# Kernel tuning notes

Hardware: AMD Instinct MI355X
Metric: run time of the kernel (lower is better)

Reference implementation:

```python
import jax, jax.numpy as jnp
import numpy as np
import math

B, LL, LP = 16, 256, 1024
HID, H = 128, 8
SCALE = math.sqrt(HID)


def setup_inputs() -> dict:
    key = jax.random.key(0)
    ks = jax.random.split(key, 20)
    s = 0.02
    inp = {
        "ligand": jax.random.normal(ks[0], (B, LL, HID), jnp.float32),
        "prot": jax.random.normal(ks[1], (B, LP, HID), jnp.float32),
        "inter": jax.random.uniform(ks[2], (B, 1, LL, LP), jnp.float32),
        # projection weights stored as [in, out] (x @ W + b)
        "Wl1": jax.random.normal(ks[3], (HID, HID * H), jnp.float32) * s,
        "bl1": jnp.zeros((HID * H,), jnp.float32),
        "Wl2": jax.random.normal(ks[4], (HID, HID * H), jnp.float32) * s,
        "bl2": jnp.zeros((HID * H,), jnp.float32),
        "Wp1": jax.random.normal(ks[5], (HID, HID * H), jnp.float32) * s,
        "bp1": jnp.zeros((HID * H,), jnp.float32),
        "Wp2": jax.random.normal(ks[6], (HID, HID * H), jnp.float32) * s,
        "bp2": jnp.zeros((HID * H,), jnp.float32),
        "W11": jax.random.normal(ks[7], (HID * H, HID), jnp.float32) * s,
        "b11": jnp.zeros((HID,), jnp.float32),
        "W12": jax.random.normal(ks[8], (2 * HID, HID), jnp.float32) * s,
        "b12": jnp.zeros((HID,), jnp.float32),
        "W21": jax.random.normal(ks[9], (HID * H, HID), jnp.float32) * s,
        "b21": jnp.zeros((HID,), jnp.float32),
        "W22": jax.random.normal(ks[10], (2 * HID, HID), jnp.float32) * s,
        "b22": jnp.zeros((HID,), jnp.float32),
    }
    return inp


def _heads(x):
    # [B, L, H*D] -> [B, H, L, D]
    b, l, _ = x.shape
    return x.reshape(b, l, H, HID).transpose(0, 2, 1, 3)


def reference(ligand, prot, inter, Wl1, bl1, Wl2, bl2, Wp1, bp1, Wp2, bp2,
              W11, b11, W12, b12, W21, b21, W22, b22):
    relu = jax.nn.relu
    l1 = _heads(relu(ligand @ Wl1 + bl1))   # [B,H,LL,D]
    l2 = _heads(relu(ligand @ Wl2 + bl2))   # [B,H,LL,D]
    p1 = _heads(relu(prot @ Wp1 + bp1))     # [B,H,LP,D]
    p2 = _heads(relu(prot @ Wp2 + bp2))     # [B,H,LP,D]

    energy = jnp.einsum('bhld,bhpd->bhlp', l1, p1) / SCALE
    att = jax.nn.softmax(energy * inter, axis=-1)  # dropout is identity at eval

    # ligand branch: att @ prot2 -> [B,LL,H*D]
    lig3 = jnp.einsum('bhlp,bhpd->blhd', att, p2).reshape(B, LL, H * HID)
    lig3 = jnp.concatenate([lig3 @ W11 + b11, ligand], axis=2)
    lig3 = relu(lig3 @ W12 + b12)

    # protein branch: att^T @ ligand2 -> [B,LP,H*D]
    prot3 = jnp.einsum('bhlp,bhld->bphd', att, l2).reshape(B, LP, H * HID)
    prot3 = jnp.concatenate([prot3 @ W21 + b21, prot], axis=2)
    prot3 = relu(prot3 @ W22 + b22)
    return (lig3, prot3)
```

## Files before the change

### kernel.cpp

```cpp
#include <hip/hip_runtime.h>
#include <hip/hip_bf16.h>

typedef unsigned short u16;
typedef __attribute__((ext_vector_type(4))) float f32x4;
typedef __attribute__((ext_vector_type(4))) unsigned int u32x4;
typedef __attribute__((ext_vector_type(4))) unsigned short u16x4;
typedef __attribute__((ext_vector_type(8))) __bf16 bf16x8;

__device__ inline float u2f(u16 u) {
    union { unsigned int i; float f; } x; x.i = ((unsigned int)u) << 16; return x.f;
}
__device__ inline u16 f2u(float f) {
    __hip_bfloat16 b = __float2bfloat16(f);
    return *reinterpret_cast<u16*>(&b);
}
__device__ inline f32x4 mfma16(bf16x8 a, bf16x8 b, f32x4 c) {
    return __builtin_amdgcn_mfma_f32_16x16x32_bf16(a, b, c, 0, 0, 0);
}
__device__ inline void gload_lds16(const u16* g, u16* l) {
    __builtin_amdgcn_global_load_lds(
        (const __attribute__((address_space(1))) unsigned int*)g,
        (__attribute__((address_space(3))) unsigned int*)l, 16, 0, 0);
}

__global__ __launch_bounds__(256)
void proj_kernel(const u16* __restrict__ ligb, const u16* __restrict__ protb,
                 const u16* __restrict__ Wl1t, const u16* __restrict__ Wl2t,
                 const u16* __restrict__ Wp1t, const u16* __restrict__ Wp2t,
                 const float* __restrict__ bl1, const float* __restrict__ bl2,
                 const float* __restrict__ bp1, const float* __restrict__ bp2,
                 u16* __restrict__ l1v, u16* __restrict__ l2tv,
                 u16* __restrict__ p1v, u16* __restrict__ p2tv)
{
    __shared__ __align__(16) u16 As[128 * 64];
    __shared__ __align__(16) u16 Bs[128 * 64];
    const int y = blockIdx.y;
    const u16* A; const u16* B; const float* bias; u16* Out;
    int mode, logL, my;
    if (y < 32)       { A = ligb;  B = Wl1t; bias = bl1; Out = l1v;  mode = 1; logL = 8;  my = y; }
    else if (y < 64)  { A = ligb;  B = Wl2t; bias = bl2; Out = l2tv; mode = 3; logL = 8;  my = y - 32; }
    else if (y < 192) { A = protb; B = Wp1t; bias = bp1; Out = p1v;  mode = 1; logL = 10; my = y - 64; }
    else              { A = protb; B = Wp2t; bias = bp2; Out = p2tv; mode = 3; logL = 10; my = y - 192; }
    const int n0 = blockIdx.x * 128, m0 = my * 128;
    const int tid = threadIdx.x;
    const int w = tid >> 6, lane = tid & 63, q = lane >> 4, li = lane & 15;
    const int wr = w >> 1, wc = w & 1;

    const int srow = tid >> 3;
    const int cg = (tid & 7) ^ (srow & 7);
    const int ldsbase = ((tid >> 6) * 8) * 64;

    f32x4 acc[4][4];
    #pragma unroll
    for (int i = 0; i < 4; i++)
        #pragma unroll
        for (int j = 0; j < 4; j++) acc[i][j] = (f32x4){0.f, 0.f, 0.f, 0.f};

    #pragma unroll
    for (int kt = 0; kt < 128; kt += 64) {
        const u16* Ab = A + (long)m0 * 128 + kt + cg * 8;
        const u16* Bb = B + (long)n0 * 128 + kt + cg * 8;
        #pragma unroll
        for (int c = 0; c < 4; c++) {
            gload_lds16(Ab + (long)(c * 32 + srow) * 128, &As[ldsbase + c * 32 * 64]);
            gload_lds16(Bb + (long)(c * 32 + srow) * 128, &Bs[ldsbase + c * 32 * 64]);
        }
        __syncthreads();
        #pragma unroll
        for (int s = 0; s < 2; s++) {
            const int cp = ((s * 4 + q) ^ (li & 7)) * 8;
            bf16x8 av[4], bv[4];
            #pragma unroll
            for (int i = 0; i < 4; i++)
                av[i] = *(bf16x8*)&As[(wr * 64 + i * 16 + li) * 64 + cp];
            #pragma unroll
            for (int j = 0; j < 4; j++)
                bv[j] = *(bf16x8*)&Bs[(wc * 64 + j * 16 + li) * 64 + cp];
            #pragma unroll
            for (int i = 0; i < 4; i++)
                #pragma unroll
                for (int j = 0; j < 4; j++)
                    acc[i][j] = mfma16(av[i], bv[j], acc[i][j]);
        }
        __syncthreads();
    }

    const int Lm = (1 << logL) - 1;
    #pragma unroll
    for (int i = 0; i < 4; i++) {
        #pragma unroll
        for (int j = 0; j < 4; j++) {
            const int col = n0 + wc * 64 + j * 16 + li;
            const float bvs = bias[col];
            if (mode == 3) {
                const int row0 = m0 + wr * 64 + i * 16 + q * 4;
                long base = ((long)(((row0 >> logL) * 8 + (col >> 7)) * 128
                            + (col & 127)) << logL) + (row0 & Lm);
                u16x4 o;
                #pragma unroll
                for (int r = 0; r < 4; r++)
                    o[r] = f2u(fmaxf(acc[i][j][r] + bvs, 0.f));
                *(u16x4*)(Out + base) = o;
            } else {
                #pragma unroll
                for (int r = 0; r < 4; r++) {
                    const int row = m0 + wr * 64 + i * 16 + q * 4 + r;
                    long addr = ((long)((row >> logL) * 8 + (col >> 7)) << (logL + 7))
                              + ((long)(row & Lm) << 7) + (col & 127);
                    Out[addr] = f2u(fmaxf(acc[i][j][r] + bvs, 0.f));
                }
            }
        }
    }
}

__global__ __launch_bounds__(512)
void av_kernel(const u16* __restrict__ att, const u16* __restrict__ p2t,
               const u16* __restrict__ l2t,
               u16* __restrict__ lig3, u16* __restrict__ prot3)
{
    __shared__ __align__(16) u16 As[256 * 64];
    __shared__ __align__(16) u16 Bs[128 * 64];
    __shared__ __align__(16) u16 T[64 * 256];
    const int bid = blockIdx.x;
    const int tid = threadIdx.x;
    const int w = tid >> 6, lane = tid & 63, q = lane >> 4, li = lane & 15;
    const int wr = w >> 1, wc = w & 1;

    f32x4 acc[4][4];
    #pragma unroll
    for (int i = 0; i < 4; i++)
        #pragma unroll
        for (int j = 0; j < 4; j++) acc[i][j] = (f32x4){0.f, 0.f, 0.f, 0.f};

    if (bid < 128) {
        const int bh = bid;
        const u16* A = att + (long)bh * 262144;
        const u16* B = p2t + (long)bh * 131072;
        const int srow = tid >> 3;
        const int cg = (tid & 7) ^ (srow & 7);
        const int ldsbase = ((tid >> 6) * 8) * 64;

        for (int kt = 0; kt < 1024; kt += 64) {
            const u16* Ab = A + kt + cg * 8;
            const u16* Bb = B + kt + cg * 8;
            #pragma unroll
            for (int c = 0; c < 4; c++)
                gload_lds16(Ab + (long)(c * 64 + srow) * 1024,
                            &As[ldsbase + c * 64 * 64]);
            #pragma unroll
            for (int c = 0; c < 2; c++)
                gload_lds16(Bb + (long)(c * 64 + srow) * 1024,
                            &Bs[ldsbase + c * 64 * 64]);
            __syncthreads();
            #pragma unroll
            for (int s = 0; s < 2; s++) {
                const int cp = ((s * 4 + q) ^ (li & 7)) * 8;
                bf16x8 av[4], bv[4];
                #pragma unroll
                for (int i = 0; i < 4; i++)
                    av[i] = *(bf16x8*)&As[(wr * 64 + i * 16 + li) * 64 + cp];
                #pragma unroll
                for (int j = 0; j < 4; j++)
                    bv[j] = *(bf16x8*)&Bs[(wc * 64 + j * 16 + li) * 64 + cp];
                #pragma unroll
                for (int i = 0; i < 4; i++)
                    #pragma unroll
                    for (int j = 0; j < 4; j++)
                        acc[i][j] = mfma16(av[i], bv[j], acc[i][j]);
            }
            __syncthreads();
        }

        const long obase = ((long)(bh >> 3) * 256) * 1024 + (long)(bh & 7) * 128;
        #pragma unroll
        for (int i = 0; i < 4; i++)
            #pragma unroll
            for (int j = 0; j < 4; j++) {
                const int col = wc * 64 + j * 16 + li;
                #pragma unroll
                for (int r = 0; r < 4; r++) {
                    const int row = wr * 64 + i * 16 + q * 4 + r;
                    lig3[obase + (long)row * 1024 + col] = f2u(acc[i][j][r]);
                }
            }
    } else {
        const int pb = bid - 128;
        const int bh = pb >> 2;
        const int m0 = (pb & 3) * 256;
        const u16* A = att + (long)bh * 262144;
        const u16* B = l2t + (long)bh * 32768;
        const int w6 = tid >> 6;
        const int i5 = (tid >> 5) & 1;
        const int srow = tid >> 3;
        const int cg = (tid & 7) ^ (srow & 7);
        const int bldsbase = w6 * 8 * 64;

        for (int kt = 0; kt < 256; kt += 64) {
            #pragma unroll
            for (int c = 0; c < 4; c++) {
                gload_lds16(A + (long)(kt + w6 * 8 + c * 2 + i5) * 1024
                              + m0 + (tid & 31) * 8,
                            &T[w6 * 2048 + c * 512]);
            }
            #pragma unroll
            for (int c = 0; c < 2; c++)
                gload_lds16(B + (long)(c * 64 + srow) * 256 + kt + cg * 8,
                            &Bs[bldsbase + c * 64 * 64]);
            __syncthreads();

            #pragma unroll
            for (int pass = 0; pass < 4; pass++) {
                const int p = pass * 64 + (tid & 63);
                union { u16 e[8]; u32x4 v; } tmp;
                #pragma unroll
                for (int e = 0; e < 8; e++)
                    tmp.e[e] = T[(w6 * 8 + e) * 256 + p];
                *(u32x4*)&As[p * 64 + ((w6 ^ (p & 7)) * 8)] = tmp.v;
            }
            __syncthreads();

            #pragma unroll
            for (int s = 0; s < 2; s++) {
                const int cp = ((s * 4 + q) ^ (li & 7)) * 8;
                bf16x8 av[4], bv[4];
                #pragma unroll
                for (int i = 0; i < 4; i++)
                    av[i] = *(bf16x8*)&As[(wr * 64 + i * 16 + li) * 64 + cp];
                #pragma unroll
                for (int j = 0; j < 4; j++)
                    bv[j] = *(bf16x8*)&Bs[(wc * 64 + j * 16 + li) * 64 + cp];
                #pragma unroll
                for (int i = 0; i < 4; i++)
                    #pragma unroll
                    for (int j = 0; j < 4; j++)
                        acc[i][j] = mfma16(av[i], bv[j], acc[i][j]);
            }
            __syncthreads();
        }

        const long obase = ((long)(bh >> 3) * 1024 + m0) * 1024 + (long)(bh & 7) * 128;
        #pragma unroll
        for (int i = 0; i < 4; i++)
            #pragma unroll
            for (int j = 0; j < 4; j++) {
                const int col = wc * 64 + j * 16 + li;
                #pragma unroll
                for (int r = 0; r < 4; r++) {
                    const int row = wr * 64 + i * 16 + q * 4 + r;
                    prot3[obase + (long)row * 1024 + col] = f2u(acc[i][j][r]);
                }
            }
    }
}

__global__ __launch_bounds__(256)
void finals_kernel(const u16* __restrict__ lig3, const u16* __restrict__ ligb,
                   const u16* __restrict__ WstL, const float* __restrict__ bcL,
                   float* __restrict__ out0,
                   const u16* __restrict__ prot3, const u16* __restrict__ protb,
                   const u16* __restrict__ WstP, const float* __restrict__ bcP,
                   float* __restrict__ out1)
{
    __shared__ __align__(16) u16 As[128 * 64];
    __shared__ __align__(16) u16 Bs[128 * 64];
    const int y = blockIdx.y;
    const u16 *A, *A2, *B; const float* bias; float* Out; int my;
    if (y < 32) { A = lig3;  A2 = ligb;  B = WstL; bias = bcL; Out = out0; my = y; }
    else        { A = prot3; A2 = protb; B = WstP; bias = bcP; Out = out1; my = y - 32; }
    const int m0 = my * 128;
    const int tid = threadIdx.x;
    const int w = tid >> 6, lane = tid & 63, q = lane >> 4, li = lane & 15;
    const int wr = w >> 1, wc = w & 1;

    const int srow = tid >> 3;
    const int cg = (tid & 7) ^ (srow & 7);
    const int ldsbase = ((tid >> 6) * 8) * 64;

    f32x4 acc[4][4];
    #pragma unroll
    for (int i = 0; i < 4; i++)
        #pragma unroll
        for (int j = 0; j < 4; j++) acc[i][j] = (f32x4){0.f, 0.f, 0.f, 0.f};

    for (int kt = 0; kt < 1152; kt += 64) {
        const u16* Abase; long lda; int ktA;
        if (kt >= 1024) { Abase = A2; lda = 128; ktA = kt - 1024; }
        else            { Abase = A;  lda = 1024; ktA = kt; }
        const u16* Ab = Abase + (long)m0 * lda + ktA + cg * 8;
        const u16* Bb = B + kt + cg * 8;
        #pragma unroll
        for (int c = 0; c < 4; c++) {
            gload_lds16(Ab + (long)(c * 32 + srow) * lda,  &As[ldsbase + c * 32 * 64]);
            gload_lds16(Bb + (long)(c * 32 + srow) * 1152, &Bs[ldsbase + c * 32 * 64]);
        }
        __syncthreads();
        #pragma unroll
        for (int s = 0; s < 2; s++) {
            const int cp = ((s * 4 + q) ^ (li & 7)) * 8;
            bf16x8 av[4], bv[4];
            #pragma unroll
            for (int i = 0; i < 4; i++)
                av[i] = *(bf16x8*)&As[(wr * 64 + i * 16 + li) * 64 + cp];
            #pragma unroll
            for (int j = 0; j < 4; j++)
                bv[j] = *(bf16x8*)&Bs[(wc * 64 + j * 16 + li) * 64 + cp];
            #pragma unroll
            for (int i = 0; i < 4; i++)
                #pragma unroll
                for (int j = 0; j < 4; j++)
                    acc[i][j] = mfma16(av[i], bv[j], acc[i][j]);
        }
        __syncthreads();
    }

    #pragma unroll
    for (int i = 0; i < 4; i++)
        #pragma unroll
        for (int j = 0; j < 4; j++) {
            const int col = wc * 64 + j * 16 + li;
            const float bvs = bias[col];
            #pragma unroll
            for (int r = 0; r < 4; r++) {
                const int row = m0 + wr * 64 + i * 16 + q * 4 + r;
                Out[(long)row * 128 + col] = fmaxf(acc[i][j][r] + bvs, 0.f);
            }
        }
}

__global__ __launch_bounds__(256)
void attn_kernel(const u16* __restrict__ l1, const u16* __restrict__ p1,
                 const float* __restrict__ inter, u16* __restrict__ att)
{
    __shared__ __align__(16) u16 As[16][136];
    __shared__ float wmax[4][16];
    __shared__ float wsum[4][16];
    const int bh = blockIdx.y;
    const int b  = bh >> 3;
    const int m0 = blockIdx.x * 16;
    const int tid = threadIdx.x;
    const int w = tid >> 6, lane = tid & 63, q = lane >> 4, li = lane & 15;

    {
        const int row = tid >> 4, col = (tid & 15) * 8;
        *(u32x4*)&As[row][col] =
            *(const u32x4*)(l1 + ((long)bh * 256 + m0 + row) * 128 + col);
    }
    __syncthreads();

    bf16x8 af[4];
    #pragma unroll
    for (int s = 0; s < 4; s++) af[s] = *(bf16x8*)&As[li][s * 32 + q * 8];

    float sv[16][4];
    const float rscale = 0.08838834764831845f;
    for (int t = 0; t < 16; t++) {
        const int n0 = w * 256 + t * 16;
        const u16* bp = p1 + ((long)bh * 1024 + n0 + li) * 128 + q * 8;
        f32x4 acc = (f32x4){0.f, 0.f, 0.f, 0.f};
        #pragma unroll
        for (int s = 0; s < 4; s++) {
            bf16x8 bfg = *(const bf16x8*)(bp + s * 32);
            acc = mfma16(af[s], bfg, acc);
        }
        const int pcol = n0 + li;
        #pragma unroll
        for (int r = 0; r < 4; r++) {
            const int l = m0 + q * 4 + r;
            float iv = inter[((long)b * 256 + l) * 1024 + pcol];
            sv[t][r] = acc[r] * rscale * iv;
        }
    }

    float rmax[4];
    #pragma unroll
    for (int r = 0; r < 4; r++) {
        float m = sv[0][r];
        #pragma unroll
        for (int t = 1; t < 16; t++) m = fmaxf(m, sv[t][r]);
        for (int d = 1; d < 16; d <<= 1) m = fmaxf(m, __shfl_xor(m, d, 64));
        rmax[r] = m;
    }
    if (li == 0) {
        #pragma unroll
        for (int r = 0; r < 4; r++) wmax[w][q * 4 + r] = rmax[r];
    }
    __syncthreads();
    float gmax[4];
    #pragma unroll
    for (int r = 0; r < 4; r++) {
        gmax[r] = fmaxf(fmaxf(wmax[0][q * 4 + r], wmax[1][q * 4 + r]),
                        fmaxf(wmax[2][q * 4 + r], wmax[3][q * 4 + r]));
    }
    #pragma unroll
    for (int r = 0; r < 4; r++) {
        float s = 0.f;
        #pragma unroll
        for (int t = 0; t < 16; t++) {
            float e = __expf(sv[t][r] - gmax[r]);
            sv[t][r] = e;
            s += e;
        }
        for (int d = 1; d < 16; d <<= 1) s += __shfl_xor(s, d, 64);
        if (li == 0) wsum[w][q * 4 + r] = s;
    }
    __syncthreads();
    float inv[4];
    #pragma unroll
    for (int r = 0; r < 4; r++) {
        float s = wsum[0][q * 4 + r] + wsum[1][q * 4 + r]
                + wsum[2][q * 4 + r] + wsum[3][q * 4 + r];
        inv[r] = 1.f / s;
    }
    for (int t = 0; t < 16; t++) {
        #pragma unroll
        for (int r = 0; r < 4; r++) {
            const int l = m0 + q * 4 + r;
            const int pcol = w * 256 + t * 16 + li;
            att[((long)bh * 256 + l) * 1024 + pcol] = f2u(sv[t][r] * inv[r]);
        }
    }
}

struct TPF { const float* src; u16* dst; int R; int C; };
struct TPF8 { TPF t[8]; };

__global__ __launch_bounds__(256)
void cvtw_kernel(TPF8 args)
{
    TPF tp = args.t[blockIdx.z];
    const int c0 = blockIdx.x * 32, r0 = blockIdx.y * 32;
    if (c0 >= tp.C || r0 >= tp.R) return;
    __shared__ u16 tile[32][33];
    const int tx = threadIdx.x & 31, ty = threadIdx.x >> 5;
    #pragma unroll
    for (int i = 0; i < 4; i++)
        tile[ty + i * 8][tx] = f2u(tp.src[(long)(r0 + ty + i * 8) * tp.C + c0 + tx]);
    __syncthreads();
    #pragma unroll
    for (int i = 0; i < 4; i++)
        tp.dst[(long)(c0 + ty + i * 8) * tp.R + r0 + tx] = tile[tx][ty + i * 8];
}

__global__ __launch_bounds__(256)
void wcomb_kernel(const u16* __restrict__ Wm0, const u16* __restrict__ Wo0,
                  const float* __restrict__ bm0, const float* __restrict__ bo0,
                  u16* __restrict__ Wst0, float* __restrict__ bc0,
                  const u16* __restrict__ Wm1, const u16* __restrict__ Wo1,
                  const float* __restrict__ bm1, const float* __restrict__ bo1,
                  u16* __restrict__ Wst1, float* __restrict__ bc1)
{
    const int zz = blockIdx.y;
    const u16* Wm = zz ? Wm1 : Wm0;
    const u16* Wo = zz ? Wo1 : Wo0;
    const float* bmid = zz ? bm1 : bm0;
    const float* bout = zz ? bo1 : bo0;
    u16* Wst = zz ? Wst1 : Wst0;
    float* bc = zz ? bc1 : bc0;
    const int n = blockIdx.x;
    const int tid = threadIdx.x;
    __shared__ float wrow[128];
    if (tid < 128) wrow[tid] = u2f(Wo[n * 256 + tid]);
    __syncthreads();
    for (int k = tid; k < 1024; k += 256) {
        float acc = 0.f;
        #pragma unroll 4
        for (int j = 0; j < 128; j++) acc += wrow[j] * u2f(Wm[(long)j * 1024 + k]);
        Wst[(long)n * 1152 + k] = f2u(acc);
    }
    if (tid < 128) Wst[(long)n * 1152 + 1024 + tid] = Wo[n * 256 + 128 + tid];
    if (tid == 0) {
        float acc = bout[n];
        for (int j = 0; j < 128; j++) acc += bmid[j] * wrow[j];
        bc[n] = acc;
    }
}

__global__ __launch_bounds__(256)
void cvt2_kernel(const float* __restrict__ a, u16* __restrict__ da, int na,
                 const float* __restrict__ b, u16* __restrict__ db, int nb)
{
    const int zz = blockIdx.y;
    const float* s = zz ? b : a;
    u16* d = zz ? db : da;
    const int n = zz ? nb : na;
    const int i = (blockIdx.x * 256 + threadIdx.x) * 4;
    if (i >= n) return;
    const float4 v = *(const float4*)(s + i);
    u16x4 o;
    o.x = f2u(v.x); o.y = f2u(v.y); o.z = f2u(v.z); o.w = f2u(v.w);
    *(u16x4*)(d + i) = o;
}

extern "C" void kernel_launch(void* const* d_in, const int* in_sizes, int n_in,
                              void* d_out, int out_size, void* d_ws, size_t ws_size,
                              hipStream_t stream)
{
    (void)in_sizes; (void)n_in; (void)out_size; (void)ws_size;
    const float* ligand = (const float*)d_in[0];
    const float* prot   = (const float*)d_in[1];
    const float* inter  = (const float*)d_in[2];
    const float* Wl1 = (const float*)d_in[3];  const float* bl1 = (const float*)d_in[4];
    const float* Wl2 = (const float*)d_in[5];  const float* bl2 = (const float*)d_in[6];
    const float* Wp1 = (const float*)d_in[7];  const float* bp1 = (const float*)d_in[8];
    const float* Wp2 = (const float*)d_in[9];  const float* bp2 = (const float*)d_in[10];
    const float* W11 = (const float*)d_in[11]; const float* b11 = (const float*)d_in[12];
    const float* W12 = (const float*)d_in[13]; const float* b12 = (const float*)d_in[14];
    const float* W21 = (const float*)d_in[15]; const float* b21 = (const float*)d_in[16];
    const float* W22 = (const float*)d_in[17]; const float* b22 = (const float*)d_in[18];

    float* out0 = (float*)d_out;
    float* out1 = out0 + (size_t)16 * 256 * 128;

    u16* ws = (u16*)d_ws;
    size_t off = 0;
    auto alloc = [&](size_t n) { u16* p = ws + off; off += n; return p; };
    u16* ligb  = alloc(524288);
    u16* protb = alloc(2097152);
    u16* l1v   = alloc(4194304);
    u16* l2t   = alloc(4194304);
    u16* p1v   = alloc(16777216);
    u16* p2t   = alloc(16777216);
    u16* attv  = alloc(33554432);
    u16* lig3  = alloc(4194304);
    u16* prot3 = alloc(16777216);
    u16* Wl1t  = alloc(131072);
    u16* Wl2t  = alloc(131072);
    u16* Wp1t  = alloc(131072);
    u16* Wp2t  = alloc(131072);
    u16* W11t  = alloc(131072);
    u16* W21t  = alloc(131072);
    u16* W12t  = alloc(32768);
    u16* W22t  = alloc(32768);
    u16* WstL  = alloc(147456);
    u16* WstP  = alloc(147456);
    float* bcL = (float*)alloc(256);
    float* bcP = (float*)alloc(256);

    cvt2_kernel<<<dim3(2048, 2), 256, 0, stream>>>(
        ligand, ligb, 524288, prot, protb, 2097152);

    TPF8 tp;
    tp.t[0] = {Wl1, Wl1t, 128, 1024};
    tp.t[1] = {Wl2, Wl2t, 128, 1024};
    tp.t[2] = {Wp1, Wp1t, 128, 1024};
    tp.t[3] = {Wp2, Wp2t, 128, 1024};
    tp.t[4] = {W11, W11t, 1024, 128};
    tp.t[5] = {W21, W21t, 1024, 128};
    tp.t[6] = {W12, W12t, 256, 128};
    tp.t[7] = {W22, W22t, 256, 128};
    cvtw_kernel<<<dim3(32, 32, 8), 256, 0, stream>>>(tp);

    wcomb_kernel<<<dim3(128, 2), 256, 0, stream>>>(
        W11t, W12t, b11, b12, WstL, bcL,
        W21t, W22t, b21, b22, WstP, bcP);

    proj_kernel<<<dim3(8, 320), 256, 0, stream>>>(
        ligb, protb, Wl1t, Wl2t, Wp1t, Wp2t,
        bl1, bl2, bp1, bp2, l1v, l2t, p1v, p2t);

    attn_kernel<<<dim3(16, 128), 256, 0, stream>>>(l1v, p1v, inter, attv);

    av_kernel<<<dim3(640), 512, 0, stream>>>(attv, p2t, l2t, lig3, prot3);

    finals_kernel<<<dim3(1, 160), 256, 0, stream>>>(
        lig3, ligb, WstL, bcL, out0,
        prot3, protb, WstP, bcP, out1);
}
```

Before: 328.0 us.

## Reuse A tile across four N tiles in proj and widen attention blocks

The projection kernel now loads the full 128x128 A tile into LDS once and loops over four 128-column weight tiles, so A reloads are cut and the grid shrinks fourfold. The attention kernel processes 32 query rows per 512-thread block instead of 16 per 256, so each block covers more rows and p1 loads are shared by the two row groups through cache. In exchange, the projection grid has fewer blocks and each block runs a serial loop with syncs. LDS use also doubles, which may lower occupancy.

```diff
diff --git a/kernel.cpp b/kernel.cpp
--- a/kernel.cpp
+++ b/kernel.cpp
@@ -32,8 +32,8 @@
                  u16* __restrict__ l1v, u16* __restrict__ l2tv,
                  u16* __restrict__ p1v, u16* __restrict__ p2tv)
 {
-    __shared__ __align__(16) u16 As[128 * 64];
-    __shared__ __align__(16) u16 Bs[128 * 64];
+    __shared__ __align__(16) u16 As[2][128 * 64];
+    __shared__ __align__(16) u16 Bs[2][128 * 64];
     const int y = blockIdx.y;
     const u16* A; const u16* B; const float* bias; u16* Out;
     int mode, logL, my;
@@ -41,76 +41,89 @@
     else if (y < 64)  { A = ligb;  B = Wl2t; bias = bl2; Out = l2tv; mode = 3; logL = 8;  my = y - 32; }
     else if (y < 192) { A = protb; B = Wp1t; bias = bp1; Out = p1v;  mode = 1; logL = 10; my = y - 64; }
     else              { A = protb; B = Wp2t; bias = bp2; Out = p2tv; mode = 3; logL = 10; my = y - 192; }
-    const int n0 = blockIdx.x * 128, m0 = my * 128;
+    const int m0 = my * 128;
+    const int nbase = blockIdx.x * 512;
     const int tid = threadIdx.x;
     const int w = tid >> 6, lane = tid & 63, q = lane >> 4, li = lane & 15;
     const int wr = w >> 1, wc = w & 1;
 
     const int srow = tid >> 3;
-    const int cg = (tid & 7) ^ (srow & 7);
+    const int cgx = (tid & 7) ^ (srow & 7);
     const int ldsbase = ((tid >> 6) * 8) * 64;
 
-    f32x4 acc[4][4];
-    #pragma unroll
-    for (int i = 0; i < 4; i++)
-        #pragma unroll
-        for (int j = 0; j < 4; j++) acc[i][j] = (f32x4){0.f, 0.f, 0.f, 0.f};
-
-    #pragma unroll
-    for (int kt = 0; kt < 128; kt += 64) {
-        const u16* Ab = A + (long)m0 * 128 + kt + cg * 8;
-        const u16* Bb = B + (long)n0 * 128 + kt + cg * 8;
-        #pragma unroll
-        for (int c = 0; c < 4; c++) {
-            gload_lds16(Ab + (long)(c * 32 + srow) * 128, &As[ldsbase + c * 32 * 64]);
-            gload_lds16(Bb + (long)(c * 32 + srow) * 128, &Bs[ldsbase + c * 32 * 64]);
+    #pragma unroll
+    for (int h = 0; h < 2; h++) {
+        const u16* Ab = A + (long)m0 * 128 + h * 64 + cgx * 8;
+        #pragma unroll
+        for (int c = 0; c < 4; c++)
+            gload_lds16(Ab + (long)(c * 32 + srow) * 128, &As[h][ldsbase + c * 32 * 64]);
+    }
+
+    const int Lm = (1 << logL) - 1;
+    for (int nt = 0; nt < 4; nt++) {
+        const int n0 = nbase + nt * 128;
+        #pragma unroll
+        for (int h = 0; h < 2; h++) {
+            const u16* Bb = B + (long)n0 * 128 + h * 64 + cgx * 8;
+            #pragma unroll
+            for (int c = 0; c < 4; c++)
+                gload_lds16(Bb + (long)(c * 32 + srow) * 128, &Bs[h][ldsbase + c * 32 * 64]);
         }
         __syncthreads();
-        #pragma unroll
-        for (int s = 0; s < 2; s++) {
-            const int cp = ((s * 4 + q) ^ (li & 7)) * 8;
-            bf16x8 av[4], bv[4];
-            #pragma unroll
-            for (int i = 0; i < 4; i++)
-                av[i] = *(bf16x8*)&As[(wr * 64 + i * 16 + li) * 64 + cp];
-            #pragma unroll
-            for (int j = 0; j < 4; j++)
-                bv[j] = *(bf16x8*)&Bs[(wc * 64 + j * 16 + li) * 64 + cp];
-            #pragma unroll
-            for (int i = 0; i < 4; i++)
+
+        f32x4 acc[4][4];
+        #pragma unroll
+        for (int i = 0; i < 4; i++)
+            #pragma unroll
+            for (int j = 0; j < 4; j++) acc[i][j] = (f32x4){0.f, 0.f, 0.f, 0.f};
+
+        #pragma unroll
+        for (int h = 0; h < 2; h++) {
+            #pragma unroll
+            for (int s = 0; s < 2; s++) {
+                const int cp = ((s * 4 + q) ^ (li & 7)) * 8;
+                bf16x8 av[4], bv[4];
+                #pragma unroll
+                for (int i = 0; i < 4; i++)
+                    av[i] = *(bf16x8*)&As[h][(wr * 64 + i * 16 + li) * 64 + cp];
                 #pragma unroll
                 for (int j = 0; j < 4; j++)
-                    acc[i][j] = mfma16(av[i], bv[j], acc[i][j]);
+                    bv[j] = *(bf16x8*)&Bs[h][(wc * 64 + j * 16 + li) * 64 + cp];
+                #pragma unroll
+                for (int i = 0; i < 4; i++)
+                    #pragma unroll
+                    for (int j = 0; j < 4; j++)
+                        acc[i][j] = mfma16(av[i], bv[j], acc[i][j]);
+            }
+        }
+
+        #pragma unroll
+        for (int i = 0; i < 4; i++) {
+            #pragma unroll
+            for (int j = 0; j < 4; j++) {
+                const int col = n0 + wc * 64 + j * 16 + li;
+                const float bvs = bias[col];
+                if (mode == 3) {
+                    const int row0 = m0 + wr * 64 + i * 16 + q * 4;
+                    long base = ((long)(((row0 >> logL) * 8 + (col >> 7)) * 128
+                                + (col & 127)) << logL) + (row0 & Lm);
+                    u16x4 o;
+                    #pragma unroll
+                    for (int r = 0; r < 4; r++)
+                        o[r] = f2u(fmaxf(acc[i][j][r] + bvs, 0.f));
+                    *(u16x4*)(Out + base) = o;
+                } else {
+                    #pragma unroll
+                    for (int r = 0; r < 4; r++) {
+                        const int row = m0 + wr * 64 + i * 16 + q * 4 + r;
+                        long addr = ((long)((row >> logL) * 8 + (col >> 7)) << (logL + 7))
+                                  + ((long)(row & Lm) << 7) + (col & 127);
+                        Out[addr] = f2u(fmaxf(acc[i][j][r] + bvs, 0.f));
+                    }
+                }
+            }
         }
         __syncthreads();
-    }
-
-    const int Lm = (1 << logL) - 1;
-    #pragma unroll
-    for (int i = 0; i < 4; i++) {
-        #pragma unroll
-        for (int j = 0; j < 4; j++) {
-            const int col = n0 + wc * 64 + j * 16 + li;
-            const float bvs = bias[col];
-            if (mode == 3) {
-                const int row0 = m0 + wr * 64 + i * 16 + q * 4;
-                long base = ((long)(((row0 >> logL) * 8 + (col >> 7)) * 128
-                            + (col & 127)) << logL) + (row0 & Lm);
-                u16x4 o;
-                #pragma unroll
-                for (int r = 0; r < 4; r++)
-                    o[r] = f2u(fmaxf(acc[i][j][r] + bvs, 0.f));
-                *(u16x4*)(Out + base) = o;
-            } else {
-                #pragma unroll
-                for (int r = 0; r < 4; r++) {
-                    const int row = m0 + wr * 64 + i * 16 + q * 4 + r;
-                    long addr = ((long)((row >> logL) * 8 + (col >> 7)) << (logL + 7))
-                              + ((long)(row & Lm) << 7) + (col & 127);
-                    Out[addr] = f2u(fmaxf(acc[i][j][r] + bvs, 0.f));
-                }
-            }
-        }
     }
 }
 
@@ -328,18 +341,19 @@
         }
 }
 
-__global__ __launch_bounds__(256)
+__global__ __launch_bounds__(512)
 void attn_kernel(const u16* __restrict__ l1, const u16* __restrict__ p1,
                  const float* __restrict__ inter, u16* __restrict__ att)
 {
-    __shared__ __align__(16) u16 As[16][136];
-    __shared__ float wmax[4][16];
-    __shared__ float wsum[4][16];
+    __shared__ __align__(16) u16 As[32][136];
+    __shared__ float wmax[8][16];
+    __shared__ float wsum[8][16];
     const int bh = blockIdx.y;
     const int b  = bh >> 3;
-    const int m0 = blockIdx.x * 16;
+    const int m0 = blockIdx.x * 32;
     const int tid = threadIdx.x;
     const int w = tid >> 6, lane = tid & 63, q = lane >> 4, li = lane & 15;
+    const int rg = w >> 2, cg = w & 3;
 
     {
         const int row = tid >> 4, col = (tid & 15) * 8;
@@ -350,12 +364,12 @@
 
     bf16x8 af[4];
     #pragma unroll
-    for (int s = 0; s < 4; s++) af[s] = *(bf16x8*)&As[li][s * 32 + q * 8];
+    for (int s = 0; s < 4; s++) af[s] = *(bf16x8*)&As[rg * 16 + li][s * 32 + q * 8];
 
     float sv[16][4];
     const float rscale = 0.08838834764831845f;
     for (int t = 0; t < 16; t++) {
-        const int n0 = w * 256 + t * 16;
+        const int n0 = cg * 256 + t * 16;
         const u16* bp = p1 + ((long)bh * 1024 + n0 + li) * 128 + q * 8;
         f32x4 acc = (f32x4){0.f, 0.f, 0.f, 0.f};
         #pragma unroll
@@ -366,31 +380,26 @@
         const int pcol = n0 + li;
         #pragma unroll
         for (int r = 0; r < 4; r++) {
-            const int l = m0 + q * 4 + r;
+            const int l = m0 + rg * 16 + q * 4 + r;
             float iv = inter[((long)b * 256 + l) * 1024 + pcol];
             sv[t][r] = acc[r] * rscale * iv;
         }
     }
 
-    float rmax[4];
     #pragma unroll
     for (int r = 0; r < 4; r++) {
         float m = sv[0][r];
         #pragma unroll
         for (int t = 1; t < 16; t++) m = fmaxf(m, sv[t][r]);
         for (int d = 1; d < 16; d <<= 1) m = fmaxf(m, __shfl_xor(m, d, 64));
-        rmax[r] = m;
-    }
-    if (li == 0) {
-        #pragma unroll
-        for (int r = 0; r < 4; r++) wmax[w][q * 4 + r] = rmax[r];
+        if (li == 0) wmax[w][q * 4 + r] = m;
     }
     __syncthreads();
     float gmax[4];
     #pragma unroll
     for (int r = 0; r < 4; r++) {
-        gmax[r] = fmaxf(fmaxf(wmax[0][q * 4 + r], wmax[1][q * 4 + r]),
-                        fmaxf(wmax[2][q * 4 + r], wmax[3][q * 4 + r]));
+        gmax[r] = fmaxf(fmaxf(wmax[rg * 4 + 0][q * 4 + r], wmax[rg * 4 + 1][q * 4 + r]),
+                        fmaxf(wmax[rg * 4 + 2][q * 4 + r], wmax[rg * 4 + 3][q * 4 + r]));
     }
     #pragma unroll
     for (int r = 0; r < 4; r++) {
@@ -408,15 +417,15 @@
     float inv[4];
     #pragma unroll
     for (int r = 0; r < 4; r++) {
-        float s = wsum[0][q * 4 + r] + wsum[1][q * 4 + r]
-                + wsum[2][q * 4 + r] + wsum[3][q * 4 + r];
+        float s = wsum[rg * 4 + 0][q * 4 + r] + wsum[rg * 4 + 1][q * 4 + r]
+                + wsum[rg * 4 + 2][q * 4 + r] + wsum[rg * 4 + 3][q * 4 + r];
         inv[r] = 1.f / s;
     }
     for (int t = 0; t < 16; t++) {
         #pragma unroll
         for (int r = 0; r < 4; r++) {
-            const int l = m0 + q * 4 + r;
-            const int pcol = w * 256 + t * 16 + li;
+            const int l = m0 + rg * 16 + q * 4 + r;
+            const int pcol = cg * 256 + t * 16 + li;
             att[((long)bh * 256 + l) * 1024 + pcol] = f2u(sv[t][r] * inv[r]);
         }
     }
@@ -555,11 +564,11 @@
         W11t, W12t, b11, b12, WstL, bcL,
         W21t, W22t, b21, b22, WstP, bcP);
 
-    proj_kernel<<<dim3(8, 320), 256, 0, stream>>>(
+    proj_kernel<<<dim3(2, 320), 256, 0, stream>>>(
         ligb, protb, Wl1t, Wl2t, Wp1t, Wp2t,
         bl1, bl2, bp1, bp2, l1v, l2t, p1v, p2t);
 
-    attn_kernel<<<dim3(16, 128), 256, 0, stream>>>(l1v, p1v, inter, attv);
+    attn_kernel<<<dim3(8, 128), 512, 0, stream>>>(l1v, p1v, inter, attv);
 
     av_kernel<<<dim3(640), 512, 0, stream>>>(attv, p2t, l2t, lig3, prot3);
 
```

Measured after the change: 339.9 us. 1.04x slower.
